# Performance work log

Hardware: AMD Instinct MI355X
Metric: run time of the kernel (lower is better)

## Reference

```python
import jax, jax.numpy as jnp
import numpy as np

DIM = 1024
HEADS = 16
DIM_HEAD = 64
INNER = HEADS * DIM_HEAD
EPS = 1e-5


def layernorm(x, g, b):
    mu = jnp.mean(x, axis=-1, keepdims=True)
    var = jnp.var(x, axis=-1, keepdims=True)
    return (x - mu) * jax.lax.rsqrt(var + EPS) * g + b


def setup_inputs() -> dict:
    key = jax.random.key(0)
    ks = jax.random.split(key, 16)
    b, n = 2, 2048
    s = 0.02
    inp = {
        "x": jax.random.normal(ks[0], (b, n, DIM), dtype=jnp.float32),
        "ln_g": jnp.ones((DIM,), jnp.float32),
        "ln_b": jnp.zeros((DIM,), jnp.float32),
        "Wq": jax.random.normal(ks[1], (DIM, INNER), jnp.float32) * s,
        "Wkv": jax.random.normal(ks[2], (DIM, 2 * DIM_HEAD), jnp.float32) * s,
        "null_kv": jax.random.normal(ks[3], (2, DIM_HEAD), jnp.float32),
        "null_attn_bias": jax.random.normal(ks[4], (HEADS,), jnp.float32),
        "pb_w0": jax.random.normal(ks[5], (1, DIM), jnp.float32) * s,
        "pb_b0": jnp.zeros((DIM,), jnp.float32),
        "pb_ln0_g": jnp.ones((DIM,), jnp.float32),
        "pb_ln0_b": jnp.zeros((DIM,), jnp.float32),
        "pb_w1": jax.random.normal(ks[6], (DIM, DIM), jnp.float32) * s,
        "pb_b1": jnp.zeros((DIM,), jnp.float32),
        "pb_ln1_g": jnp.ones((DIM,), jnp.float32),
        "pb_ln1_b": jnp.zeros((DIM,), jnp.float32),
        "pb_w2": jax.random.normal(ks[7], (DIM, HEADS), jnp.float32) * s,
        "pb_b2": jnp.zeros((HEADS,), jnp.float32),
        "Wo": jax.random.normal(ks[8], (INNER, DIM), jnp.float32) * s,
        "out_ln_g": jnp.ones((DIM,), jnp.float32),
        "out_ln_b": jnp.zeros((DIM,), jnp.float32),
    }
    return inp


def dynamic_pos_bias(n, pb_w0, pb_b0, pb_ln0_g, pb_ln0_b, pb_w1, pb_b1,
                     pb_ln1_g, pb_ln1_b, pb_w2, pb_b2):
    # pos in [-(n-1), n-1], shape [2n-1, 1]
    pos = jnp.arange(-n + 1, n, dtype=jnp.float32)[:, None]
    h = jax.nn.silu(layernorm(pos @ pb_w0 + pb_b0, pb_ln0_g, pb_ln0_b))
    h = jax.nn.silu(layernorm(h @ pb_w1 + pb_b1, pb_ln1_g, pb_ln1_b))
    h = h @ pb_w2 + pb_b2  # [2n-1, heads]
    i = jnp.arange(n)
    idx = i[:, None] - i[None, :] + (n - 1)  # [n, n]
    bias = h[idx]  # [n, n, heads]
    return jnp.transpose(bias, (2, 0, 1))  # [heads, n, n]


def attention_fwd(x, ln_g, ln_b, Wq, Wkv, null_kv, null_attn_bias,
                  pb_w0, pb_b0, pb_ln0_g, pb_ln0_b, pb_w1, pb_b1,
                  pb_ln1_g, pb_ln1_b, pb_w2, pb_b2, Wo, out_ln_g, out_ln_b):
    b, n, _ = x.shape
    scale = DIM_HEAD ** -0.5
    xn = layernorm(x, ln_g, ln_b)
    q = (xn @ Wq).reshape(b, n, HEADS, DIM_HEAD).transpose(0, 2, 1, 3) * scale  # [b,h,n,d]
    kv = xn @ Wkv  # [b,n,2d]
    k, v = kv[..., :DIM_HEAD], kv[..., DIM_HEAD:]  # single-head MQA kv
    nk = jnp.broadcast_to(null_kv[0], (b, 1, DIM_HEAD))
    nv = jnp.broadcast_to(null_kv[1], (b, 1, DIM_HEAD))
    k = jnp.concatenate([nk, k], axis=1)  # [b, n+1, d]
    v = jnp.concatenate([nv, v], axis=1)
    sim = jnp.einsum('bhid,bjd->bhij', q, k)  # [b,h,n,n+1]
    rel = dynamic_pos_bias(n, pb_w0, pb_b0, pb_ln0_g, pb_ln0_b,
                           pb_w1, pb_b1, pb_ln1_g, pb_ln1_b, pb_w2, pb_b2)
    null_bias = jnp.broadcast_to(null_attn_bias[:, None, None], (HEADS, n, 1))
    attn_bias = jnp.concatenate([null_bias, rel], axis=-1)  # [h, n, n+1]
    sim = sim + attn_bias[None]
    max_neg = -jnp.finfo(sim.dtype).max
    causal_mask = jnp.triu(jnp.ones((n, n + 1), dtype=bool), k=2)
    sim = jnp.where(causal_mask[None, None], max_neg, sim)
    attn = jax.nn.softmax(sim, axis=-1)
    out = jnp.einsum('bhij,bjd->bhid', attn, v)  # [b,h,n,d]
    out = out.transpose(0, 2, 1, 3).reshape(b, n, INNER)
    return layernorm(out @ Wo, out_ln_g, out_ln_b)


def reference(x, ln_g, ln_b, Wq, Wkv, null_kv, null_attn_bias,
              pb_w0, pb_b0, pb_ln0_g, pb_ln0_b, pb_w1, pb_b1,
              pb_ln1_g, pb_ln1_b, pb_w2, pb_b2, Wo, out_ln_g, out_ln_b):
    return attention_fwd(x, ln_g, ln_b, Wq, Wkv, null_kv, null_attn_bias,
                         pb_w0, pb_b0, pb_ln0_g, pb_ln0_b, pb_w1, pb_b1,
                         pb_ln1_g, pb_ln1_b, pb_w2, pb_b2, Wo, out_ln_g, out_ln_b)
```

## Files before the change

kernel.cpp:

```cpp
#include <hip/hip_runtime.h>
#include <hip/hip_bf16.h>
#include <math.h>

#define DIMM   1024
#define NHEADS 16
#define DHEAD  64
#define BATCH  2
#define SEQ    2048
#define NKEYS  (SEQ + 1)
#define NKROWS 2112
#define NKP    2112
#define PBROWS (2 * SEQ - 1)
#define ROWS   (BATCH * SEQ)

using bf16x8 = __attribute__((ext_vector_type(8))) short;
using f32x4  = __attribute__((ext_vector_type(4))) float;
typedef unsigned int u32;
typedef unsigned short u16;

__device__ __forceinline__ u16 f2bf(float f) {
  __hip_bfloat16 h = __float2bfloat16(f);
  return __builtin_bit_cast(u16, h);
}
__device__ __forceinline__ float bf2f(u16 u) {
  u32 x = ((u32)u) << 16;
  return __builtin_bit_cast(float, x);
}
__device__ __forceinline__ void gl_lds16(const void* g, void* l) {
  __builtin_amdgcn_global_load_lds(
      (const __attribute__((address_space(1))) u32*)g,
      (__attribute__((address_space(3))) u32*)l, 16, 0, 0);
}

__global__ __launch_bounds__(256) void ln_kernel(
    const float* __restrict__ in, const float* __restrict__ addb,
    const float* __restrict__ g, const float* __restrict__ bvec,
    void* __restrict__ outv, int silu, int obf16, int posrow) {
  int row = blockIdx.x;
  int t = threadIdx.x;
  float4 x;
  if (posrow) {
    float p = (float)(row - (SEQ - 1));
    float4 wv = ((const float4*)in)[t];
    float4 a = ((const float4*)addb)[t];
    x.x = p * wv.x + a.x; x.y = p * wv.y + a.y;
    x.z = p * wv.z + a.z; x.w = p * wv.w + a.w;
  } else {
    x = ((const float4*)(in + (size_t)row * DIMM))[t];
    if (addb) {
      float4 a = ((const float4*)addb)[t];
      x.x += a.x; x.y += a.y; x.z += a.z; x.w += a.w;
    }
  }
  float s  = x.x + x.y + x.z + x.w;
  float ss = x.x * x.x + x.y * x.y + x.z * x.z + x.w * x.w;
#pragma unroll
  for (int off = 32; off > 0; off >>= 1) {
    s  += __shfl_down(s, off);
    ss += __shfl_down(ss, off);
  }
  __shared__ float rs[4], rss[4];
  int wv_ = t >> 6, lane = t & 63;
  if (lane == 0) { rs[wv_] = s; rss[wv_] = ss; }
  __syncthreads();
  float S  = rs[0] + rs[1] + rs[2] + rs[3];
  float SS = rss[0] + rss[1] + rss[2] + rss[3];
  float mu  = S * (1.0f / DIMM);
  float var = SS * (1.0f / DIMM) - mu * mu;
  float inv = rsqrtf(var + 1e-5f);
  float4 gv = ((const float4*)g)[t];
  float4 bv = ((const float4*)bvec)[t];
  float4 o;
  o.x = (x.x - mu) * inv * gv.x + bv.x;
  o.y = (x.y - mu) * inv * gv.y + bv.y;
  o.z = (x.z - mu) * inv * gv.z + bv.z;
  o.w = (x.w - mu) * inv * gv.w + bv.w;
  if (silu) {
    o.x = o.x / (1.f + expf(-o.x));
    o.y = o.y / (1.f + expf(-o.y));
    o.z = o.z / (1.f + expf(-o.z));
    o.w = o.w / (1.f + expf(-o.w));
  }
  if (obf16) {
    ushort4 ob;
    ob.x = f2bf(o.x); ob.y = f2bf(o.y); ob.z = f2bf(o.z); ob.w = f2bf(o.w);
    ((ushort4*)((u16*)outv + (size_t)row * DIMM))[t] = ob;
  } else {
    ((float4*)((float*)outv + (size_t)row * DIMM))[t] = o;
  }
}

__global__ __launch_bounds__(256) void conv_wT(
    const float* __restrict__ W, u16* __restrict__ WT, int N, int rowOff) {
  __shared__ float tile[32][33];
  const int n0 = blockIdx.x * 32, k0 = blockIdx.y * 32;
  const int tc = threadIdx.x & 31, tr = threadIdx.x >> 5;
#pragma unroll
  for (int i = 0; i < 4; ++i)
    tile[tr + i * 8][tc] = W[(size_t)(k0 + tr + i * 8) * N + n0 + tc];
  __syncthreads();
#pragma unroll
  for (int i = 0; i < 4; ++i) {
    int r = tr + i * 8;
    WT[(size_t)(rowOff + n0 + r) * 1024 + k0 + tc] = f2bf(tile[tc][r]);
  }
}

__global__ __launch_bounds__(256) void gemm_bf16(
    const u16* __restrict__ A, const u16* __restrict__ BT,
    float* __restrict__ C, int M, int N, int K) {
  __shared__ u16 As[128 * 32];
  __shared__ u16 Bs[128 * 32];
  const int w = threadIdx.x >> 6, lane = threadIdx.x & 63;
  const int lo = lane & 15, hi = lane >> 4;
  const int wr = w >> 1, wc = w & 1;
  const int row0 = blockIdx.y * 128, col0 = blockIdx.x * 128;
  const int srow = lane >> 2;
  const int scol = (lane & 3) * 8;
  f32x4 acc[4][4];
#pragma unroll
  for (int m = 0; m < 4; ++m)
#pragma unroll
    for (int n = 0; n < 4; ++n) acc[m][n] = f32x4{0.f, 0.f, 0.f, 0.f};
  for (int k0 = 0; k0 < K; k0 += 32) {
#pragma unroll
    for (int c = 0; c < 2; ++c) {
      const int base = 32 * w + c * 16;
      gl_lds16(A + (size_t)(row0 + base + srow) * K + k0 + scol,
               &As[base * 32]);
      gl_lds16(BT + (size_t)(col0 + base + srow) * K + k0 + scol,
               &Bs[base * 32]);
    }
    __syncthreads();
    bf16x8 af[4], bg[4];
#pragma unroll
    for (int m = 0; m < 4; ++m)
      af[m] = *(const bf16x8*)&As[(wr * 64 + m * 16 + lo) * 32 + hi * 8];
#pragma unroll
    for (int n = 0; n < 4; ++n)
      bg[n] = *(const bf16x8*)&Bs[(wc * 64 + n * 16 + lo) * 32 + hi * 8];
#pragma unroll
    for (int m = 0; m < 4; ++m)
#pragma unroll
      for (int n = 0; n < 4; ++n)
        acc[m][n] = __builtin_amdgcn_mfma_f32_16x16x32_bf16(af[m], bg[n],
                                                            acc[m][n], 0, 0, 0);
    __syncthreads();
  }
#pragma unroll
  for (int m = 0; m < 4; ++m)
#pragma unroll
    for (int r = 0; r < 4; ++r) {
      const int row = row0 + wr * 64 + m * 16 + hi * 4 + r;
      if (row < M) {
#pragma unroll
        for (int n = 0; n < 4; ++n)
          C[(size_t)row * N + col0 + wc * 64 + n * 16 + lo] = acc[m][n][r];
      }
    }
}

__global__ __launch_bounds__(256) void relayout_q(
    const float* __restrict__ tmp, u16* __restrict__ qb) {
  size_t e = (size_t)blockIdx.x * 256 + threadIdx.x;
  int m = (int)(e >> 8), c4 = (int)(e & 255);
  int b = m >> 11, i = m & 2047;
  int h = c4 >> 4, d4 = c4 & 15;
  float4 v = ((const float4*)(tmp + (size_t)m * 1152))[c4];
  const float sc = 0.125f;
  ushort4 o;
  o.x = f2bf(v.x * sc); o.y = f2bf(v.y * sc);
  o.z = f2bf(v.z * sc); o.w = f2bf(v.w * sc);
  ((ushort4*)qb)[((size_t)(b * NHEADS + h) * SEQ + i) * 16 + d4] = o;
}

__global__ __launch_bounds__(256) void relayout_kv(
    const float* __restrict__ tmp, u16* __restrict__ kb, u16* __restrict__ vbT) {
  size_t e = (size_t)blockIdx.x * 256 + threadIdx.x;
  int m = (int)(e >> 5), c4 = (int)(e & 31);
  int b = m >> 11, i = m & 2047;
  float4 v = ((const float4*)(tmp + (size_t)m * 1152 + 1024))[c4];
  if (c4 < 16) {
    ushort4 o;
    o.x = f2bf(v.x); o.y = f2bf(v.y); o.z = f2bf(v.z); o.w = f2bf(v.w);
    ((ushort4*)kb)[((size_t)b * NKROWS + (i + 1)) * 16 + c4] = o;
  } else {
    int d = (c4 - 16) * 4;
    size_t base = (size_t)b * DHEAD * NKP + (size_t)d * NKP + (i + 1);
    vbT[base]           = f2bf(v.x);
    vbT[base + NKP]     = f2bf(v.y);
    vbT[base + 2 * NKP] = f2bf(v.z);
    vbT[base + 3 * NKP] = f2bf(v.w);
  }
}

__global__ void fill_null(const float* __restrict__ null_kv,
                          u16* __restrict__ kb, u16* __restrict__ vbT) {
  int b = blockIdx.x, d = threadIdx.x;
  kb[(size_t)b * NKROWS * DHEAD + d] = f2bf(null_kv[d]);
  vbT[(size_t)b * DHEAD * NKP + (size_t)d * NKP] = f2bf(null_kv[DHEAD + d]);
}

__global__ __launch_bounds__(256) void h2_kernel(
    const u16* __restrict__ h1, const float* __restrict__ w2,
    const float* __restrict__ b2, float* __restrict__ bias_tabT) {
  int r = blockIdx.x, t = threadIdx.x;
  int col = t & 15, seg = t >> 4;
  const u16* hr = h1 + (size_t)r * DIMM;
  float acc = 0.f;
  for (int k = seg * 64; k < seg * 64 + 64; ++k)
    acc += bf2f(hr[k]) * w2[(size_t)k * NHEADS + col];
  __shared__ float p[16][16];
  p[seg][col] = acc;
  __syncthreads();
  if (t < 16) {
    float s = 0.f;
#pragma unroll
    for (int q = 0; q < 16; q++) s += p[q][t];
    bias_tabT[(size_t)t * 4096 + r] = s + b2[t];
  }
}

__global__ __launch_bounds__(256, 4) void flash_attn(
    const u16* __restrict__ qb, const u16* __restrict__ kb,
    const u16* __restrict__ vbT, const float* __restrict__ bias_tabT,
    const float* __restrict__ null_bias, u16* __restrict__ outb) {
  const int qt = gridDim.x - 1 - blockIdx.x;
  const int h = blockIdx.y, b = blockIdx.z;
  const int w = threadIdx.x >> 6, lane = threadIdx.x & 63;
  const int lo = lane & 15, hi = lane >> 4;
  const int q0 = qt * 64, r0 = w * 16;
  const int rq = q0 + r0 + lo;

  __shared__ u16 plds[4][16][72];

  const u16* qrow = qb + (size_t)((b * NHEADS + h) * SEQ + rq) * DHEAD;
  bf16x8 qa0 = *(const bf16x8*)(qrow + hi * 8);
  bf16x8 qa1 = *(const bf16x8*)(qrow + 32 + hi * 8);

  const u16* Kb = kb + (size_t)b * NKROWS * DHEAD;
  const u16* Vb = vbT + (size_t)b * DHEAD * NKP;
  const float* bt = bias_tabT + (size_t)h * 4096;
  const float nb = null_bias[h];

  f32x4 o[4];
#pragma unroll
  for (int nf = 0; nf < 4; ++nf) o[nf] = f32x4{0.f, 0.f, 0.f, 0.f};
  float m_l = -3.0e38f, l_l = 0.f;

  const int nkt = qt + 2;
  for (int kt = 0; kt < nkt; ++kt) {
    const int j0 = kt * 64;
    bf16x8 kf0[4], kf1[4];
#pragma unroll
    for (int nf = 0; nf < 4; ++nf) {
      const u16* krow = Kb + (size_t)(j0 + nf * 16 + lo) * DHEAD;
      kf0[nf] = *(const bf16x8*)(krow + hi * 8);
      kf1[nf] = *(const bf16x8*)(krow + 32 + hi * 8);
    }
    float bias[4][4];
#pragma unroll
    for (int nf = 0; nf < 4; ++nf)
#pragma unroll
      for (int r = 0; r < 4; ++r) {
        const int key = j0 + nf * 16 + hi * 4 + r;
        bias[nf][r] = (key == 0) ? nb : bt[rq - key + SEQ];
      }
    f32x4 s[4];
#pragma unroll
    for (int nf = 0; nf < 4; ++nf) {
      f32x4 acc = f32x4{0.f, 0.f, 0.f, 0.f};
      acc = __builtin_amdgcn_mfma_f32_16x16x32_bf16(kf0[nf], qa0, acc, 0, 0, 0);
      acc = __builtin_amdgcn_mfma_f32_16x16x32_bf16(kf1[nf], qa1, acc, 0, 0, 0);
      s[nf] = acc;
    }
    bf16x8 vf0[4], vf1[4];
#pragma unroll
    for (int nf = 0; nf < 4; ++nf) {
      const u16* vrow = Vb + (size_t)(nf * 16 + lo) * NKP + j0;
      vf0[nf] = *(const bf16x8*)(vrow + hi * 8);
      vf1[nf] = *(const bf16x8*)(vrow + 32 + hi * 8);
    }
    float tm = -3.0e38f;
#pragma unroll
    for (int nf = 0; nf < 4; ++nf)
#pragma unroll
      for (int r = 0; r < 4; ++r) {
        const int key = j0 + nf * 16 + hi * 4 + r;
        float v = (key <= rq + 1) ? (s[nf][r] + bias[nf][r]) : -3.0e38f;
        s[nf][r] = v;
        tm = fmaxf(tm, v);
      }
    tm = fmaxf(tm, __shfl_xor(tm, 16));
    tm = fmaxf(tm, __shfl_xor(tm, 32));
    if (__any(tm > m_l + 8.0f)) {
      float mn = fmaxf(m_l, tm);
      float sco = __expf(m_l - mn);
      m_l = mn;
      l_l *= sco;
      float scoq[4];
#pragma unroll
      for (int r = 0; r < 4; ++r) scoq[r] = __shfl(sco, hi * 4 + r);
#pragma unroll
      for (int nf = 0; nf < 4; ++nf)
#pragma unroll
        for (int r = 0; r < 4; ++r) o[nf][r] *= scoq[r];
    }
#pragma unroll
    for (int nf = 0; nf < 4; ++nf) {
      float p0 = __expf(s[nf][0] - m_l);
      float p1 = __expf(s[nf][1] - m_l);
      float p2 = __expf(s[nf][2] - m_l);
      float p3 = __expf(s[nf][3] - m_l);
      l_l += (p0 + p1) + (p2 + p3);
      uint2 pk;
      pk.x = (u32)f2bf(p0) | ((u32)f2bf(p1) << 16);
      pk.y = (u32)f2bf(p2) | ((u32)f2bf(p3) << 16);
      *(uint2*)&plds[w][lo][nf * 16 + hi * 4] = pk;
    }
    bf16x8 pa0 = *(const bf16x8*)&plds[w][lo][hi * 8];
    bf16x8 pa1 = *(const bf16x8*)&plds[w][lo][32 + hi * 8];
#pragma unroll
    for (int nf = 0; nf < 4; ++nf) {
      o[nf] = __builtin_amdgcn_mfma_f32_16x16x32_bf16(pa0, vf0[nf], o[nf], 0, 0, 0);
      o[nf] = __builtin_amdgcn_mfma_f32_16x16x32_bf16(pa1, vf1[nf], o[nf], 0, 0, 0);
    }
  }
  float lf = l_l;
  lf += __shfl_xor(lf, 16);
  lf += __shfl_xor(lf, 32);
  float linv = 1.0f / lf;
  float linvq[4];
#pragma unroll
  for (int r = 0; r < 4; ++r) linvq[r] = __shfl(linv, hi * 4 + r);
#pragma unroll
  for (int nf = 0; nf < 4; ++nf)
#pragma unroll
    for (int r = 0; r < 4; ++r) {
      const int row = q0 + r0 + hi * 4 + r;
      outb[(size_t)(b * SEQ + row) * DIMM + h * DHEAD + nf * 16 + lo] =
          f2bf(o[nf][r] * linvq[r]);
    }
}

extern "C" void kernel_launch(void* const* d_in, const int* in_sizes, int n_in,
                              void* d_out, int out_size, void* d_ws,
                              size_t ws_size, hipStream_t stream) {
  const float* x         = (const float*)d_in[0];
  const float* ln_g      = (const float*)d_in[1];
  const float* ln_b      = (const float*)d_in[2];
  const float* Wq        = (const float*)d_in[3];
  const float* Wkv       = (const float*)d_in[4];
  const float* null_kv   = (const float*)d_in[5];
  const float* null_bias = (const float*)d_in[6];
  const float* pb_w0     = (const float*)d_in[7];
  const float* pb_b0     = (const float*)d_in[8];
  const float* pb_ln0_g  = (const float*)d_in[9];
  const float* pb_ln0_b  = (const float*)d_in[10];
  const float* pb_w1     = (const float*)d_in[11];
  const float* pb_b1     = (const float*)d_in[12];
  const float* pb_ln1_g  = (const float*)d_in[13];
  const float* pb_ln1_b  = (const float*)d_in[14];
  const float* pb_w2     = (const float*)d_in[15];
  const float* pb_b2     = (const float*)d_in[16];
  const float* Wo        = (const float*)d_in[17];
  const float* out_ln_g  = (const float*)d_in[18];
  const float* out_ln_b  = (const float*)d_in[19];
  float* out = (float*)d_out;

  char* ws = (char*)d_ws;
  float* regA      = (float*)(ws);
  u16*   h1_bf     = (u16*)(ws + 18874368);
  u16*   regC      = (u16*)(ws + 35651584);
  u16*   qb        = (u16*)(ws + 44040192);
  u16*   kb        = (u16*)(ws + 52428800);
  u16*   vbT       = (u16*)(ws + 52969472);
  u16*   wqkvT     = (u16*)(ws + 53510144);
  u16*   w1T       = (u16*)(ws + 55869440);
  u16*   woT       = (u16*)(ws + 57966592);
  float* bias_tabT = (float*)(ws + 60063744);

  hipMemsetAsync((void*)kb, 0, 1081344, stream);

  conv_wT<<<dim3(32, 32), 256, 0, stream>>>(Wq, wqkvT, 1024, 0);
  conv_wT<<<dim3(4, 32), 256, 0, stream>>>(Wkv, wqkvT, 128, 1024);
  conv_wT<<<dim3(32, 32), 256, 0, stream>>>(pb_w1, w1T, 1024, 0);
  conv_wT<<<dim3(32, 32), 256, 0, stream>>>(Wo, woT, 1024, 0);

  ln_kernel<<<ROWS, 256, 0, stream>>>(x, nullptr, ln_g, ln_b, regC, 0, 1, 0);
  gemm_bf16<<<dim3(9, 32), 256, 0, stream>>>(regC, wqkvT, regA, ROWS, 1152,
                                             1024);
  relayout_q<<<4096, 256, 0, stream>>>(regA, qb);
  relayout_kv<<<512, 256, 0, stream>>>(regA, kb, vbT);
  fill_null<<<2, 64, 0, stream>>>(null_kv, kb, vbT);
  ln_kernel<<<PBROWS, 256, 0, stream>>>(pb_w0, pb_b0, pb_ln0_g, pb_ln0_b, regC,
                                        1, 1, 1);
  gemm_bf16<<<dim3(8, 32), 256, 0, stream>>>(regC, w1T, regA, PBROWS, 1024,
                                             1024);
  ln_kernel<<<PBROWS, 256, 0, stream>>>(regA, pb_b1, pb_ln1_g, pb_ln1_b, h1_bf,
                                        1, 1, 0);
  h2_kernel<<<PBROWS, 256, 0, stream>>>(h1_bf, pb_w2, pb_b2, bias_tabT);
  flash_attn<<<dim3(SEQ / 64, NHEADS, BATCH), 256, 0, stream>>>(
      qb, kb, vbT, bias_tabT, null_bias, regC);
  gemm_bf16<<<dim3(8, 32), 256, 0, stream>>>(regC, woT, regA, ROWS, 1024, 1024);
  ln_kernel<<<ROWS, 256, 0, stream>>>(regA, nullptr, out_ln_g, out_ln_b, out, 0,
                                      0, 0);
}
```

Measured before the change: 499.7 us.

## Keep P in registers via transposed PV MFMA, prefetch K, vectorize bias loads

Reformulates the P·V product as V^T·P^T using 16x16x16 MFMAs so the softmax probabilities stay in registers in their native layout, removing the LDS round trip and the shuffles for rescaling and normalization. K fragments for the next tile are prefetched during the current tile's softmax. Bias values are loaded as one unaligned float4 read in reversed order, with a special case for the null key. MFMA blocks are wrapped in s_setprio, and the output is written as 4-wide vectors. Register pressure goes up and the inline asm MFMA needs manual nop hazard padding.

Measured after the change: 614.0 us. +22.9%, slower.

```diff
diff --git a/kernel.cpp b/kernel.cpp
--- a/kernel.cpp
+++ b/kernel.cpp
@@ -14,7 +14,9 @@
 #define ROWS   (BATCH * SEQ)
 
 using bf16x8 = __attribute__((ext_vector_type(8))) short;
+using bf16x4 = __attribute__((ext_vector_type(4))) short;
 using f32x4  = __attribute__((ext_vector_type(4))) float;
+typedef float f32x4u __attribute__((ext_vector_type(4), aligned(4)));
 typedef unsigned int u32;
 typedef unsigned short u16;
 
@@ -30,6 +32,10 @@
   __builtin_amdgcn_global_load_lds(
       (const __attribute__((address_space(1))) u32*)g,
       (__attribute__((address_space(3))) u32*)l, 16, 0, 0);
+}
+__device__ __forceinline__ f32x4 mfma16(bf16x4 a, bf16x4 b, f32x4 c) {
+  asm("v_mfma_f32_16x16x16_bf16 %0, %1, %2, %0" : "+v"(c) : "v"(a), "v"(b));
+  return c;
 }
 
 __global__ __launch_bounds__(256) void ln_kernel(
@@ -232,8 +238,6 @@
   const int q0 = qt * 64, r0 = w * 16;
   const int rq = q0 + r0 + lo;
 
-  __shared__ u16 plds[4][16][72];
-
   const u16* qrow = qb + (size_t)((b * NHEADS + h) * SEQ + rq) * DHEAD;
   bf16x8 qa0 = *(const bf16x8*)(qrow + hi * 8);
   bf16x8 qa1 = *(const bf16x8*)(qrow + 32 + hi * 8);
@@ -245,28 +249,36 @@
 
   f32x4 o[4];
 #pragma unroll
-  for (int nf = 0; nf < 4; ++nf) o[nf] = f32x4{0.f, 0.f, 0.f, 0.f};
+  for (int dc = 0; dc < 4; ++dc) o[dc] = f32x4{0.f, 0.f, 0.f, 0.f};
   float m_l = -3.0e38f, l_l = 0.f;
 
   const int nkt = qt + 2;
+  bf16x8 kf0[4], kf1[4];
+#pragma unroll
+  for (int nf = 0; nf < 4; ++nf) {
+    const u16* krow = Kb + (size_t)(nf * 16 + lo) * DHEAD;
+    kf0[nf] = *(const bf16x8*)(krow + hi * 8);
+    kf1[nf] = *(const bf16x8*)(krow + 32 + hi * 8);
+  }
+
   for (int kt = 0; kt < nkt; ++kt) {
     const int j0 = kt * 64;
-    bf16x8 kf0[4], kf1[4];
-#pragma unroll
-    for (int nf = 0; nf < 4; ++nf) {
-      const u16* krow = Kb + (size_t)(j0 + nf * 16 + lo) * DHEAD;
-      kf0[nf] = *(const bf16x8*)(krow + hi * 8);
-      kf1[nf] = *(const bf16x8*)(krow + 32 + hi * 8);
-    }
-    float bias[4][4];
+    bf16x4 vf[4][4];
+#pragma unroll
+    for (int dc = 0; dc < 4; ++dc) {
+      const u16* vrow = Vb + (size_t)(dc * 16 + lo) * NKP + j0 + hi * 4;
+#pragma unroll
+      for (int kc = 0; kc < 4; ++kc)
+        vf[dc][kc] = *(const bf16x4*)(vrow + kc * 16);
+    }
+    f32x4u bias[4];
 #pragma unroll
     for (int nf = 0; nf < 4; ++nf)
-#pragma unroll
-      for (int r = 0; r < 4; ++r) {
-        const int key = j0 + nf * 16 + hi * 4 + r;
-        bias[nf][r] = (key == 0) ? nb : bt[rq - key + SEQ];
-      }
+      bias[nf] =
+          *(const f32x4u*)(bt + (rq - (j0 + nf * 16 + hi * 4 + 3) + SEQ));
+    if (j0 == 0 && hi == 0) bias[0][3] = nb;
     f32x4 s[4];
+    __builtin_amdgcn_s_setprio(1);
 #pragma unroll
     for (int nf = 0; nf < 4; ++nf) {
       f32x4 acc = f32x4{0.f, 0.f, 0.f, 0.f};
@@ -274,12 +286,15 @@
       acc = __builtin_amdgcn_mfma_f32_16x16x32_bf16(kf1[nf], qa1, acc, 0, 0, 0);
       s[nf] = acc;
     }
-    bf16x8 vf0[4], vf1[4];
-#pragma unroll
-    for (int nf = 0; nf < 4; ++nf) {
-      const u16* vrow = Vb + (size_t)(nf * 16 + lo) * NKP + j0;
-      vf0[nf] = *(const bf16x8*)(vrow + hi * 8);
-      vf1[nf] = *(const bf16x8*)(vrow + 32 + hi * 8);
+    __builtin_amdgcn_s_setprio(0);
+    {
+      const int jn = (kt + 1 < nkt ? kt + 1 : kt) * 64;
+#pragma unroll
+      for (int nf = 0; nf < 4; ++nf) {
+        const u16* krow = Kb + (size_t)(jn + nf * 16 + lo) * DHEAD;
+        kf0[nf] = *(const bf16x8*)(krow + hi * 8);
+        kf1[nf] = *(const bf16x8*)(krow + 32 + hi * 8);
+      }
     }
     float tm = -3.0e38f;
 #pragma unroll
@@ -287,7 +302,7 @@
 #pragma unroll
       for (int r = 0; r < 4; ++r) {
         const int key = j0 + nf * 16 + hi * 4 + r;
-        float v = (key <= rq + 1) ? (s[nf][r] + bias[nf][r]) : -3.0e38f;
+        float v = (key <= rq + 1) ? (s[nf][r] + bias[nf][3 - r]) : -3.0e38f;
         s[nf][r] = v;
         tm = fmaxf(tm, v);
       }
@@ -298,14 +313,12 @@
       float sco = __expf(m_l - mn);
       m_l = mn;
       l_l *= sco;
-      float scoq[4];
-#pragma unroll
-      for (int r = 0; r < 4; ++r) scoq[r] = __shfl(sco, hi * 4 + r);
-#pragma unroll
-      for (int nf = 0; nf < 4; ++nf)
-#pragma unroll
-        for (int r = 0; r < 4; ++r) o[nf][r] *= scoq[r];
-    }
+#pragma unroll
+      for (int dc = 0; dc < 4; ++dc)
+#pragma unroll
+        for (int r = 0; r < 4; ++r) o[dc][r] *= sco;
+    }
+    bf16x4 pb[4];
 #pragma unroll
     for (int nf = 0; nf < 4; ++nf) {
       float p0 = __expf(s[nf][0] - m_l);
@@ -313,34 +326,33 @@
       float p2 = __expf(s[nf][2] - m_l);
       float p3 = __expf(s[nf][3] - m_l);
       l_l += (p0 + p1) + (p2 + p3);
-      uint2 pk;
-      pk.x = (u32)f2bf(p0) | ((u32)f2bf(p1) << 16);
-      pk.y = (u32)f2bf(p2) | ((u32)f2bf(p3) << 16);
-      *(uint2*)&plds[w][lo][nf * 16 + hi * 4] = pk;
-    }
-    bf16x8 pa0 = *(const bf16x8*)&plds[w][lo][hi * 8];
-    bf16x8 pa1 = *(const bf16x8*)&plds[w][lo][32 + hi * 8];
-#pragma unroll
-    for (int nf = 0; nf < 4; ++nf) {
-      o[nf] = __builtin_amdgcn_mfma_f32_16x16x32_bf16(pa0, vf0[nf], o[nf], 0, 0, 0);
-      o[nf] = __builtin_amdgcn_mfma_f32_16x16x32_bf16(pa1, vf1[nf], o[nf], 0, 0, 0);
-    }
-  }
+      pb[nf][0] = (short)f2bf(p0);
+      pb[nf][1] = (short)f2bf(p1);
+      pb[nf][2] = (short)f2bf(p2);
+      pb[nf][3] = (short)f2bf(p3);
+    }
+    __builtin_amdgcn_s_setprio(1);
+#pragma unroll
+    for (int dc = 0; dc < 4; ++dc)
+#pragma unroll
+      for (int kc = 0; kc < 4; ++kc) o[dc] = mfma16(vf[dc][kc], pb[kc], o[dc]);
+    __builtin_amdgcn_s_setprio(0);
+  }
+  asm volatile("s_nop 7\n\ts_nop 7" :::);
   float lf = l_l;
   lf += __shfl_xor(lf, 16);
   lf += __shfl_xor(lf, 32);
   float linv = 1.0f / lf;
-  float linvq[4];
-#pragma unroll
-  for (int r = 0; r < 4; ++r) linvq[r] = __shfl(linv, hi * 4 + r);
-#pragma unroll
-  for (int nf = 0; nf < 4; ++nf)
-#pragma unroll
-    for (int r = 0; r < 4; ++r) {
-      const int row = q0 + r0 + hi * 4 + r;
-      outb[(size_t)(b * SEQ + row) * DIMM + h * DHEAD + nf * 16 + lo] =
-          f2bf(o[nf][r] * linvq[r]);
-    }
+  u16* orow = outb + (size_t)(b * SEQ + rq) * DIMM + h * DHEAD + hi * 4;
+#pragma unroll
+  for (int dc = 0; dc < 4; ++dc) {
+    ushort4 st;
+    st.x = f2bf(o[dc][0] * linv);
+    st.y = f2bf(o[dc][1] * linv);
+    st.z = f2bf(o[dc][2] * linv);
+    st.w = f2bf(o[dc][3] * linv);
+    *(ushort4*)(orow + dc * 16) = st;
+  }
 }
 
 extern "C" void kernel_launch(void* const* d_in, const int* in_sizes, int n_in,
```
